# Performance work log

Measured on AMD Instinct MI355X. Metric: run time of the kernel, lower is better.

## Reference

```python
import jax, jax.numpy as jnp
import numpy as np
import math

B, C_LOW, C_HIGH, H, W = 8, 128, 256, 128, 128
KS = 7

def _conv(x, w, b, pad):
    out = jax.lax.conv_general_dilated(
        x, w, window_strides=(1, 1), padding=[(pad, pad), (pad, pad)],
        dimension_numbers=('NCHW', 'OIHW', 'NCHW'))
    return out + b[None, :, None, None]

def setup_inputs() -> dict:
    key = jax.random.key(0)
    ks = jax.random.split(key, 6)
    def he(k, shape):  # matches torch init: normal(0, sqrt(2/(kh*kw*out)))
        n = shape[2] * shape[3] * shape[0]
        return jax.random.normal(k, shape, jnp.float32) * math.sqrt(2.0 / n)
    return {
        'cur_low': jax.random.normal(ks[0], (B, C_LOW, H, W), jnp.float32),
        'key_low': jax.random.normal(ks[1], (B, C_LOW, H, W), jnp.float32),
        'key_high': jax.random.normal(ks[2], (B, C_HIGH, H, W), jnp.float32),
        'w_red': he(ks[3], (256, C_LOW, 3, 3)),
        'b_red': jnp.zeros((256,), jnp.float32),
        'w2': he(ks[4], (256, 512, 3, 3)),
        'b2': jnp.zeros((256,), jnp.float32),
        'w3': he(ks[5], (KS * KS, 256, 1, 1)),
        'b3': jnp.zeros((KS * KS,), jnp.float32),
    }

def reference(cur_low, key_low, key_high, w_red, b_red, w2, b2, w3, b3):
    # KernelWeightPredictor
    cur = jax.nn.relu(_conv(cur_low, w_red, b_red, 1))
    key = jax.nn.relu(_conv(key_low, w_red, b_red, 1))
    x = jax.nn.relu(_conv(jnp.concatenate([cur, key], axis=1), w2, b2, 1))
    x = jax.nn.relu(_conv(x, w3, b3, 0))            # [B, k*k, H, W]
    x = jax.nn.softmax(x, axis=1)
    b, k2, h, w = x.shape
    kernels = jnp.transpose(x, (0, 2, 3, 1)).reshape(b, h, w, KS, KS)
    # SpatiallyVariantConvolution: per-pixel 7x7 kernel applied to key_high
    pad = KS // 2
    fp = jnp.pad(key_high, ((0, 0), (0, 0), (pad, pad), (pad, pad)))
    out = jnp.zeros_like(key_high)
    for i in range(KS):          # fixed 49-iteration unrolled loop; avoids
        for j in range(KS):      # materializing the [B,C,H,W,K,K] patch tensor
            out = out + fp[:, :, i:i + h, j:j + w] * kernels[:, None, :, :, i, j]
    return out
```

## Files before the change

### kernel.cpp

```cpp
#include <hip/hip_runtime.h>
#include <stdint.h>
#include <stddef.h>

#define BN   8
#define HN   128
#define WN   128
#define HP   130
#define CLOW 128
#define CMID 256
#define KO   49

#define KHB_H 134
#define KHB_W 144
#define KHB_PLANE (KHB_H * KHB_W)

typedef __attribute__((ext_vector_type(4))) float f32x4;
typedef __attribute__((ext_vector_type(8))) short bf16x8;

typedef __attribute__((address_space(1))) const uint8_t ga_u8;
typedef __attribute__((address_space(3))) uint8_t lds_u8;

__device__ __forceinline__ short f2bf(float f) {
    uint32_t u = __float_as_uint(f);
    u += 0x7fffu + ((u >> 16) & 1u);
    return (short)(u >> 16);
}
__device__ __forceinline__ float bf2f(short s) {
    return __uint_as_float(((uint32_t)(uint16_t)s) << 16);
}
__device__ __forceinline__ void gload16(const void* g, void* l) {
    __builtin_amdgcn_global_load_lds((ga_u8*)g, (lds_u8*)l, 16, 0, 0);
}

__global__ __launch_bounds__(256) void zero_border_all_kernel(
    short* __restrict__ b0, short* __restrict__ b1,
    short* __restrict__ b2, short* __restrict__ b3) {
    const int which = blockIdx.y;
    short* buf = (which == 0) ? b0 : (which == 1) ? b1 : (which == 2) ? b2 : b3;
    const int gsh = (which < 2) ? 4 : 5;
    const int C = (which < 2) ? 128 : 256;
    int t = blockIdx.x * 256 + threadIdx.x;
    int cell = t >> gsh, g = t & ((1 << gsh) - 1);
    if (cell >= 8 * 516) return;
    int b = cell / 516, r = cell - b * 516;
    int y, x;
    if (r < 260) { y = (r >= 130) ? 129 : 0; x = (r >= 130) ? (r - 130) : r; }
    else { int j = r - 260; y = 1 + (j >> 1); x = (j & 1) ? 129 : 0; }
    uint4 z = {0u, 0u, 0u, 0u};
    *(uint4*)&buf[(((size_t)b * HP + y) * HP + x) * C + g * 8] = z;
}

__global__ __launch_bounds__(256) void convert_pad_kernel(
    const float* __restrict__ src0, const float* __restrict__ src1,
    short* __restrict__ dst0, short* __restrict__ dst1) {
    __shared__ short t[128 * 136];
    const int tid = threadIdx.x;
    const int by = blockIdx.x;
    const int b = by >> 7, y = by & 127;
    const float* src = blockIdx.y ? src1 : src0;
    short* dst = blockIdx.y ? dst1 : dst0;
    #pragma unroll
    for (int k = 0; k < 16; ++k) {
        int slot = k * 256 + tid;
        int c = slot >> 5, xg = slot & 31;
        f32x4 v = *(const f32x4*)&src[(((size_t)b * CLOW + c) * HN + y) * WN + xg * 4];
        #pragma unroll
        for (int j = 0; j < 4; ++j) t[(xg * 4 + j) * 136 + c] = f2bf(v[j]);
    }
    __syncthreads();
    short* drow = dst + (((size_t)b * HP + (y + 1)) * HP + 1) * CLOW;
    #pragma unroll
    for (int k = 0; k < 8; ++k) {
        int slot = k * 256 + tid;
        int x = slot >> 4, cg = slot & 15;
        *(bf16x8*)&drow[x * CLOW + cg * 8] = *(const bf16x8*)&t[x * 136 + cg * 8];
    }
}

__global__ __launch_bounds__(256) void pack_w_all_kernel(
    const float* __restrict__ w1, short* __restrict__ wp1,
    const float* __restrict__ w2, short* __restrict__ wp2,
    const float* __restrict__ w3, short* __restrict__ wp3) {
    int i = blockIdx.x * 256 + threadIdx.x;
    if (i < 256 * 1152 + 256 * 4608) {
        const float* w; short* wp; int CIN, K;
        if (i < 256 * 1152) { w = w1; wp = wp1; CIN = 128; K = 1152; }
        else { i -= 256 * 1152; w = w2; wp = wp2; CIN = 512; K = 4608; }
        int cout = i / K;
        int r = i - cout * K;
        int t = r >> 6;
        int j = r & 63;
        int cb = t / 9;
        int tap = t - cb * 9;
        int cin = cb * 64 + j;
        wp[i] = f2bf(w[((size_t)cout * CIN + cin) * 9 + tap]);
    } else {
        int j = i - (256 * 1152 + 256 * 4608);
        if (j >= 64 * 256) return;
        int o = j >> 8, ch = j & 255;
        wp3[j] = (o < KO) ? f2bf(w3[o * 256 + ch]) : (short)0;
    }
}

template <int CIN, bool OPAD, bool FUSE>
__global__ __launch_bounds__(512, 2) void conv_8ph_kernel(
    const short* __restrict__ in_a, const short* __restrict__ in_b,
    const short* __restrict__ wp, const float* __restrict__ bias,
    short* __restrict__ out_a, short* __restrict__ out_b,
    const short* __restrict__ w3p, const float* __restrict__ b3,
    float* __restrict__ z) {
    constexpr int K = 9 * CIN;
    constexpr int NT = K / 64;
    constexpr bool DUAL = (CIN == 512);
    constexpr int PST = DUAL ? 256 : CIN;
    extern __shared__ __align__(16) short lds[];
    const int tid = threadIdx.x;
    int bx = blockIdx.x;
    bx = (bx & 7) * 64 + (bx >> 3);
    const int b = bx >> 6, y0 = (bx & 63) << 1;
    const short* inA = DUAL ? in_a : (blockIdx.z ? in_b : in_a);
    const short* inB = DUAL ? in_b : inA;
    short* out = (!DUAL && blockIdx.z) ? out_b : out_a;

    const int lane = tid & 63, wv = tid >> 6;
    const int wm = wv >> 2, wn = wv & 3;
    const int lr = lane & 15, lk = lane >> 4;

    const int rA = tid >> 3, cc = tid & 7;
    const int cs = cc ^ (rA & 7);
    const int pthrA0 = rA * PST + cs * 8;
    const int pthrA1 = (rA + 64) * PST + cs * 8;
    const int pthrB0 = rA * K + cs * 8;
    const int pthrB1 = (rA + 64) * K + cs * 8;
    const int dA0 = rA * 64 + cc * 8;
    const int dB0 = rA * 64 + cc * 8;

    const int arow = (wm * 128 + lr) * 64;
    const int brow = (wn * 64 + lr) * 64;
    const int cof0 = ((lk) ^ (lr & 7)) * 8;
    const int cof1 = ((4 + lk) ^ (lr & 7)) * 8;

    f32x4 acc[8][4];
    f32x4 zero = {0.f, 0.f, 0.f, 0.f};
    #pragma unroll
    for (int i = 0; i < 8; ++i)
        #pragma unroll
        for (int j = 0; j < 4; ++j) acc[i][j] = zero;

    auto STAGE2 = [&](int t2, int which, short* bufA, short* bufB) {
        const int cb = (t2 * 57) >> 9;
        const int tap = t2 - cb * 9;
        const int ch0v = cb << 6;
        const short* src = (!DUAL || ch0v < 256) ? inA : inB;
        const int ch0 = DUAL ? (ch0v & 255) : ch0v;
        const int ky = (tap * 11) >> 5;
        const int kx = tap - ky * 3;
        if (which == 0 || which == 2) {
            const int po = (which == 0) ? pthrA0 : pthrA1;
            const int doff = (which == 0) ? 0 : 64 * 64;
            const short* s0 = src + ((size_t)(b * HP + (y0 + ky)) * HP + kx) * PST + ch0;
            gload16(s0 + po, bufA + doff + dA0);
            gload16(s0 + (HP * PST) + po, bufA + 128 * 64 + doff + dA0);
        } else {
            const int h2 = (which == 1) ? 0 : 1;
            const short* sb = wp + (size_t)(h2 * 128) * K + t2 * 64;
            short* d = bufB + h2 * 128 * 64 + dB0;
            gload16(sb + pthrB0, d);
            gload16(sb + pthrB1, d + 64 * 64);
        }
    };

    auto LDA = [&](const short* bufA, int mh, bf16x8 (&a)[4][2]) {
        #pragma unroll
        for (int i = 0; i < 4; ++i) {
            const int ro = arow + (mh * 64 + i * 16) * 64;
            a[i][0] = *(const bf16x8*)(bufA + ro + cof0);
            a[i][1] = *(const bf16x8*)(bufA + ro + cof1);
        }
    };
    auto LDB = [&](const short* bufB, int nh, bf16x8 (&bb)[2][2]) {
        #pragma unroll
        for (int j = 0; j < 2; ++j) {
            const int ro = brow + (nh * 32 + j * 16) * 64;
            bb[j][0] = *(const bf16x8*)(bufB + ro + cof0);
            bb[j][1] = *(const bf16x8*)(bufB + ro + cof1);
        }
    };

#define PH_PRE4() do { __builtin_amdgcn_sched_barrier(0); \
                       __builtin_amdgcn_s_barrier(); \
                       asm volatile("s_waitcnt lgkmcnt(4)" ::: "memory"); \
                       __builtin_amdgcn_sched_barrier(0); \
                       __builtin_amdgcn_s_setprio(1); } while (0)
#define PH_PRE() do { __builtin_amdgcn_sched_barrier(0); \
                      __builtin_amdgcn_s_barrier(); \
                      asm volatile("s_waitcnt lgkmcnt(0)" ::: "memory"); \
                      __builtin_amdgcn_sched_barrier(0); \
                      __builtin_amdgcn_s_setprio(1); } while (0)
#define PH_POST() do { __builtin_amdgcn_s_setprio(0); \
                       __builtin_amdgcn_sched_barrier(0); \
                       __builtin_amdgcn_s_barrier(); } while (0)
#define MFMA_Q(A_, B_, MH, NH) do { \
    _Pragma("unroll") \
    for (int i_ = 0; i_ < 4; ++i_) { \
        _Pragma("unroll") \
        for (int j_ = 0; j_ < 2; ++j_) { \
            acc[(MH)*4+i_][(NH)*2+j_] = __builtin_amdgcn_mfma_f32_16x16x32_bf16( \
                A_[i_][0], B_[j_][0], acc[(MH)*4+i_][(NH)*2+j_], 0, 0, 0); \
            acc[(MH)*4+i_][(NH)*2+j_] = __builtin_amdgcn_mfma_f32_16x16x32_bf16( \
                A_[i_][1], B_[j_][1], acc[(MH)*4+i_][(NH)*2+j_], 0, 0, 0); \
        } \
    } } while (0)

    short* const A0 = lds;
    short* const A1 = lds + 16384;
    short* const B0 = lds + 32768;
    short* const B1 = lds + 49152;

    STAGE2(0, 0, A0, B0); STAGE2(0, 1, A0, B0);
    STAGE2(0, 2, A0, B0); STAGE2(0, 3, A0, B0);
    STAGE2(1, 0, A1, B1); STAGE2(1, 1, A1, B1);
    STAGE2(1, 2, A1, B1); STAGE2(1, 3, A1, B1);
    asm volatile("s_waitcnt vmcnt(8)" ::: "memory");
    __builtin_amdgcn_sched_barrier(0);
    __builtin_amdgcn_s_barrier();

    auto TILE = [&](int t, short* bufA, short* bufB) {
        const int t2 = t + 2;
        const bool st = (t2 < NT);
        bf16x8 ar[4][2], br0[2][2], br1[2][2];
        LDA(bufA, 0, ar);
        LDB(bufB, 0, br0);
        LDB(bufB, 1, br1);
        if (st) STAGE2(t2, 0, bufA, bufB);
        PH_PRE4();
        MFMA_Q(ar, br0, 0, 0);
        PH_POST();
        if (st) STAGE2(t2, 1, bufA, bufB);
        PH_PRE();
        MFMA_Q(ar, br1, 0, 1);
        PH_POST();
        LDA(bufA, 1, ar);
        if (st) STAGE2(t2, 2, bufA, bufB);
        PH_PRE();
        MFMA_Q(ar, br0, 1, 0);
        PH_POST();
        if (st) STAGE2(t2, 3, bufA, bufB);
        PH_PRE();
        MFMA_Q(ar, br1, 1, 1);
        __builtin_amdgcn_s_setprio(0);
        __builtin_amdgcn_sched_barrier(0);
        if (st)                asm volatile("s_waitcnt vmcnt(8)" ::: "memory");
        else if (t == NT - 2)  asm volatile("s_waitcnt vmcnt(0)" ::: "memory");
        __builtin_amdgcn_sched_barrier(0);
        __builtin_amdgcn_s_barrier();
    };

    for (int t = 0; t < NT; t += 2) {
        TILE(t,     A0, B0);
        TILE(t + 1, A1, B1);
    }
#undef PH_PRE4
#undef PH_PRE
#undef PH_POST
#undef MFMA_Q

    float bvs[4];
    #pragma unroll
    for (int nf = 0; nf < 4; ++nf) bvs[nf] = bias[wn * 64 + nf * 16 + lr];

    if constexpr (!FUSE) {
        #pragma unroll
        for (int mf = 0; mf < 8; ++mf) {
            #pragma unroll
            for (int rr = 0; rr < 4; ++rr) {
                const int p = wm * 128 + mf * 16 + lk * 4 + rr;
                const int y = y0 + (p >> 7), x = p & 127;
                short* op;
                if (OPAD)
                    op = out + ((size_t)(b * HP + (y + 1)) * HP + (x + 1)) * CMID + wn * 64 + lr;
                else
                    op = out + ((size_t)((b * HN + y) * WN + x)) * CMID + wn * 64 + lr;
                #pragma unroll
                for (int nf = 0; nf < 4; ++nf)
                    op[nf * 16] = f2bf(fmaxf(acc[mf][nf][rr] + bvs[nf], 0.f));
            }
        }
    } else {
        short* const Xh  = lds;
        short* const W3s = lds + 32768;

        #pragma unroll
        for (int sweep = 0; sweep < 4; ++sweep) {
            const int s = sweep * 512 + tid;
            const int o = s >> 5, c = s & 31;
            gload16(w3p + o * 256 + ((c ^ (o & 7)) << 3), W3s + s * 8);
        }

        const int oo = wn * 16 + lr;
        const float b3v = (oo < KO) ? b3[oo] : 0.f;

        #pragma unroll 1
        for (int r = 0; r < 2; ++r) {
            if (wm == r) {
                #pragma unroll
                for (int nf = 0; nf < 4; ++nf) {
                    const int ch = wn * 64 + nf * 16 + lr;
                    const int ck = ch >> 3, el = ch & 7;
                    #pragma unroll
                    for (int mf = 0; mf < 8; ++mf) {
                        #pragma unroll
                        for (int rr = 0; rr < 4; ++rr) {
                            const int px = mf * 16 + lk * 4 + rr;
                            Xh[px * 256 + ((ck ^ (px & 7)) << 3) + el] =
                                f2bf(fmaxf(acc[mf][nf][rr] + bvs[nf], 0.f));
                        }
                    }
                }
            }
            __syncthreads();
            f32x4 a2[4];
            #pragma unroll
            for (int m = 0; m < 4; ++m) {
                a2[m][0] = b3v; a2[m][1] = b3v; a2[m][2] = b3v; a2[m][3] = b3v;
            }
            #pragma unroll
            for (int ks = 0; ks < 8; ++ks) {
                const bf16x8 bfr =
                    *(const bf16x8*)&W3s[oo * 256 + (((ks * 4 + lk) ^ (oo & 7)) << 3)];
                #pragma unroll
                for (int m = 0; m < 4; ++m) {
                    const int px = wm * 64 + m * 16 + lr;
                    const bf16x8 afr =
                        *(const bf16x8*)&Xh[px * 256 + (((ks * 4 + lk) ^ (px & 7)) << 3)];
                    a2[m] = __builtin_amdgcn_mfma_f32_16x16x32_bf16(afr, bfr, a2[m], 0, 0, 0);
                }
            }
            float* zp = z + ((size_t)(b * 16384 + (y0 + r) * 128)) * 64;
            #pragma unroll
            for (int m = 0; m < 4; ++m) {
                #pragma unroll
                for (int r2 = 0; r2 < 4; ++r2) {
                    const int px = wm * 64 + m * 16 + lk * 4 + r2;
                    zp[px * 64 + oo] = a2[m][r2];
                }
            }
            if (r == 0) __syncthreads();
        }
    }
}

__global__ __launch_bounds__(256) void pad_kh_kernel(
    const float* __restrict__ kh, short* __restrict__ khb) {
    const int bc = blockIdx.x;
    const float* src = kh + (size_t)bc * (HN * WN);
    short* dst = khb + (size_t)bc * KHB_PLANE;
    for (int i = threadIdx.x; i < KHB_H * (KHB_W / 8); i += 256) {
        int yy = i / (KHB_W / 8);
        int g = i - yy * (KHB_W / 8);
        int ys = yy - 3;
        bf16x8 v;
        #pragma unroll
        for (int t = 0; t < 8; ++t) {
            int xs = g * 8 + t - 4;
            float f = 0.f;
            if ((unsigned)ys < 128u && (unsigned)xs < 128u) f = src[(ys << 7) + xs];
            v[t] = f2bf(f);
        }
        *(bf16x8*)&dst[yy * KHB_W + g * 8] = v;
    }
}

__global__ __launch_bounds__(256) void svc4_kernel(
    const float* __restrict__ z, const short* __restrict__ khb,
    float* __restrict__ out) {
    __shared__ float a_s[KO * 64];
    const int tid = threadIdx.x;
    int by = blockIdx.y;
    by = (by & 7) * 128 + (by >> 3);
    const int b = by >> 7, y = by & 127;
    const int x0 = blockIdx.x * 64;

    {
        const int px = tid >> 2, l = tid & 3;
        const float* zp = z + ((size_t)(b * 16384 + (y << 7) + x0 + px)) * 64 + l * 16;
        float v[16];
        #pragma unroll
        for (int q = 0; q < 4; ++q) {
            f32x4 t4 = *(const f32x4*)&zp[q * 4];
            v[q * 4 + 0] = fmaxf(t4[0], 0.f);
            v[q * 4 + 1] = fmaxf(t4[1], 0.f);
            v[q * 4 + 2] = fmaxf(t4[2], 0.f);
            v[q * 4 + 3] = fmaxf(t4[3], 0.f);
        }
        #pragma unroll
        for (int j = 1; j < 16; ++j) if (l == 3) v[j] = -1e30f;
        float m = v[0];
        #pragma unroll
        for (int j = 1; j < 16; ++j) m = fmaxf(m, v[j]);
        m = fmaxf(m, __shfl_xor(m, 1, 64));
        m = fmaxf(m, __shfl_xor(m, 2, 64));
        float s = 0.f;
        #pragma unroll
        for (int j = 0; j < 16; ++j) { v[j] = __expf(v[j] - m); s += v[j]; }
        s += __shfl_xor(s, 1, 64);
        s += __shfl_xor(s, 2, 64);
        const float inv = 1.f / s;
        #pragma unroll
        for (int j = 0; j < 16; ++j) {
            const int o = l * 16 + j;
            if (o < KO) a_s[o * 64 + px] = v[j] * inv;
        }
    }
    __syncthreads();

    const int ci = tid >> 3;
    const int pg = tid & 7;
    const int p0 = x0 + pg * 8;

    float acc[8][8];
    #pragma unroll
    for (int c = 0; c < 8; ++c)
        #pragma unroll
        for (int j = 0; j < 8; ++j) acc[c][j] = 0.f;

    const short* kbase = khb + (((size_t)b * 256 + ci) * KHB_H + y) * KHB_W + p0;

    #pragma unroll 1
    for (int dy = 0; dy < 7; ++dy) {
        f32x4 av[14];
        #pragma unroll
        for (int dx = 0; dx < 7; ++dx) {
            av[dx * 2]     = *(const f32x4*)&a_s[(dy * 7 + dx) * 64 + pg * 8];
            av[dx * 2 + 1] = *(const f32x4*)&a_s[(dy * 7 + dx) * 64 + pg * 8 + 4];
        }
        const short* krow = kbase + dy * KHB_W;
        #pragma unroll
        for (int c = 0; c < 8; ++c) {
            const short* kp = krow + (size_t)c * 32 * KHB_PLANE;
            bf16x8 k0 = *(const bf16x8*)(kp);
            bf16x8 k1 = *(const bf16x8*)(kp + 8);
            float win[16];
            #pragma unroll
            for (int t = 0; t < 8; ++t) { win[t] = bf2f(k0[t]); win[t + 8] = bf2f(k1[t]); }
            #pragma unroll
            for (int dx = 0; dx < 7; ++dx) {
                #pragma unroll
                for (int j = 0; j < 8; ++j)
                    acc[c][j] = fmaf(win[j + dx + 1], av[dx * 2 + (j >> 2)][j & 3],
                                     acc[c][j]);
            }
        }
    }

    #pragma unroll
    for (int c = 0; c < 8; ++c) {
        float* op = out + (((size_t)b * 256 + ci + c * 32) << 14) + (y << 7) + p0;
        f32x4 r0 = {acc[c][0], acc[c][1], acc[c][2], acc[c][3]};
        f32x4 r1 = {acc[c][4], acc[c][5], acc[c][6], acc[c][7]};
        *(f32x4*)op = r0;
        *(f32x4*)(op + 4) = r1;
    }
}

extern "C" void kernel_launch(void* const* d_in, const int* in_sizes, int n_in,
                              void* d_out, int out_size, void* d_ws, size_t ws_size,
                              hipStream_t stream) {
    (void)in_sizes; (void)n_in; (void)out_size; (void)ws_size;
    const float* cur_low  = (const float*)d_in[0];
    const float* key_low  = (const float*)d_in[1];
    const float* key_high = (const float*)d_in[2];
    const float* w_red    = (const float*)d_in[3];
    const float* b_red    = (const float*)d_in[4];
    const float* w2       = (const float*)d_in[5];
    const float* b2       = (const float*)d_in[6];
    const float* w3       = (const float*)d_in[7];
    const float* b3       = (const float*)d_in[8];
    float* out = (float*)d_out;
    char* ws = (char*)d_ws;

    const size_t SZ_XPAD = (size_t)BN * HP * HP * CLOW * 2;
    const size_t SZ_YPAD = (size_t)BN * HP * HP * CMID * 2;
    short* xpadc = (short*)(ws);
    short* xpadk = (short*)(ws + SZ_XPAD);
    short* ypadc = (short*)(ws + 2 * SZ_XPAD);
    short* ypadk = (short*)(ws + 2 * SZ_XPAD + SZ_YPAD);
    short* w1p   = (short*)(ws + 2 * SZ_XPAD + 2 * SZ_YPAD);
    short* w2p   = w1p + (size_t)256 * 1152;
    float* z     = (float*)(ws);
    short* khb   = (short*)(ws + 2 * SZ_XPAD);
    short* w3p   = (short*)((char*)d_out + (size_t)134217728 - 32768);

    hipFuncSetAttribute((const void*)conv_8ph_kernel<128, true, false>,
                        hipFuncAttributeMaxDynamicSharedMemorySize, 131072);
    hipFuncSetAttribute((const void*)conv_8ph_kernel<512, false, true>,
                        hipFuncAttributeMaxDynamicSharedMemorySize, 131072);

    zero_border_all_kernel<<<dim3(516, 4), 256, 0, stream>>>(xpadc, xpadk, ypadc, ypadk);
    convert_pad_kernel<<<dim3(1024, 2), 256, 0, stream>>>(cur_low, key_low, xpadc, xpadk);
    pack_w_all_kernel<<<(256 * (1152 + 4608) + 64 * 256 + 255) / 256, 256, 0, stream>>>(
        w_red, w1p, w2, w2p, w3, w3p);

    conv_8ph_kernel<128, true, false><<<dim3(512, 1, 2), 512, 131072, stream>>>(
        xpadc, xpadk, w1p, b_red, ypadc, ypadk, nullptr, nullptr, nullptr);

    conv_8ph_kernel<512, false, true><<<dim3(512, 1, 1), 512, 131072, stream>>>(
        ypadc, ypadk, w2p, b2, nullptr, nullptr, w3p, b3, z);

    pad_kh_kernel<<<2048, 256, 0, stream>>>(key_high, khb);
    svc4_kernel<<<dim3(2, 1024), 256, 0, stream>>>(z, khb, out);
}
```

Before: 654.5 us.

## Replace ping-pong phased GEMM pipeline with simple one-tile-ahead double buffering

Restructures the MFMA main loop. It drops the 4-phase interleaved schedule, where each tile issued staged global loads for tile t+2 between MFMA quarters with barriers around each phase. The new loop issues all loads for tile t+1 into the other buffer at the start of each tile, waits once, and then runs all MFMAs with only two barriers per tile. This removes six barriers per tile but prefetches only one tile ahead, so global load latency is less hidden behind compute. A __syncthreads is added before the fused epilogue reuses LDS.

```diff
diff --git a/kernel.cpp b/kernel.cpp
--- a/kernel.cpp
+++ b/kernel.cpp
@@ -187,19 +187,6 @@
         }
     };
 
-#define PH_PRE4() do { __builtin_amdgcn_sched_barrier(0); \
-                       __builtin_amdgcn_s_barrier(); \
-                       asm volatile("s_waitcnt lgkmcnt(4)" ::: "memory"); \
-                       __builtin_amdgcn_sched_barrier(0); \
-                       __builtin_amdgcn_s_setprio(1); } while (0)
-#define PH_PRE() do { __builtin_amdgcn_sched_barrier(0); \
-                      __builtin_amdgcn_s_barrier(); \
-                      asm volatile("s_waitcnt lgkmcnt(0)" ::: "memory"); \
-                      __builtin_amdgcn_sched_barrier(0); \
-                      __builtin_amdgcn_s_setprio(1); } while (0)
-#define PH_POST() do { __builtin_amdgcn_s_setprio(0); \
-                       __builtin_amdgcn_sched_barrier(0); \
-                       __builtin_amdgcn_s_barrier(); } while (0)
 #define MFMA_Q(A_, B_, MH, NH) do { \
     _Pragma("unroll") \
     for (int i_ = 0; i_ < 4; ++i_) { \
@@ -219,50 +206,42 @@
 
     STAGE2(0, 0, A0, B0); STAGE2(0, 1, A0, B0);
     STAGE2(0, 2, A0, B0); STAGE2(0, 3, A0, B0);
-    STAGE2(1, 0, A1, B1); STAGE2(1, 1, A1, B1);
-    STAGE2(1, 2, A1, B1); STAGE2(1, 3, A1, B1);
-    asm volatile("s_waitcnt vmcnt(8)" ::: "memory");
-    __builtin_amdgcn_sched_barrier(0);
-    __builtin_amdgcn_s_barrier();
-
-    auto TILE = [&](int t, short* bufA, short* bufB) {
-        const int t2 = t + 2;
-        const bool st = (t2 < NT);
+
+    auto TILE = [&](int t, short* bufA, short* bufB, short* nA, short* nB) {
+        __builtin_amdgcn_s_barrier();
+        __builtin_amdgcn_sched_barrier(0);
+        const int t1 = t + 1;
+        if (t1 < NT) {
+            STAGE2(t1, 0, nA, nB); STAGE2(t1, 1, nA, nB);
+            STAGE2(t1, 2, nA, nB); STAGE2(t1, 3, nA, nB);
+            __builtin_amdgcn_sched_barrier(0);
+            asm volatile("s_waitcnt vmcnt(8)" ::: "memory");
+        } else {
+            __builtin_amdgcn_sched_barrier(0);
+            asm volatile("s_waitcnt vmcnt(0)" ::: "memory");
+        }
+        __builtin_amdgcn_sched_barrier(0);
+        __builtin_amdgcn_s_barrier();
+        __builtin_amdgcn_sched_barrier(0);
         bf16x8 ar[4][2], br0[2][2], br1[2][2];
         LDA(bufA, 0, ar);
         LDB(bufB, 0, br0);
         LDB(bufB, 1, br1);
-        if (st) STAGE2(t2, 0, bufA, bufB);
-        PH_PRE4();
+        __builtin_amdgcn_s_setprio(1);
         MFMA_Q(ar, br0, 0, 0);
-        PH_POST();
-        if (st) STAGE2(t2, 1, bufA, bufB);
-        PH_PRE();
         MFMA_Q(ar, br1, 0, 1);
-        PH_POST();
+        __builtin_amdgcn_s_setprio(0);
         LDA(bufA, 1, ar);
-        if (st) STAGE2(t2, 2, bufA, bufB);
-        PH_PRE();
+        __builtin_amdgcn_s_setprio(1);
         MFMA_Q(ar, br0, 1, 0);
-        PH_POST();
-        if (st) STAGE2(t2, 3, bufA, bufB);
-        PH_PRE();
         MFMA_Q(ar, br1, 1, 1);
         __builtin_amdgcn_s_setprio(0);
-        __builtin_amdgcn_sched_barrier(0);
-        if (st)                asm volatile("s_waitcnt vmcnt(8)" ::: "memory");
-        else if (t == NT - 2)  asm volatile("s_waitcnt vmcnt(0)" ::: "memory");
-        __builtin_amdgcn_sched_barrier(0);
-        __builtin_amdgcn_s_barrier();
     };
 
     for (int t = 0; t < NT; t += 2) {
-        TILE(t,     A0, B0);
-        TILE(t + 1, A1, B1);
-    }
-#undef PH_PRE4
-#undef PH_PRE
-#undef PH_POST
+        TILE(t,     A0, B0, A1, B1);
+        TILE(t + 1, A1, B1, A0, B0);
+    }
 #undef MFMA_Q
 
     float bvs[4];
@@ -287,6 +266,7 @@
             }
         }
     } else {
+        __syncthreads();
         short* const Xh  = lds;
         short* const W3s = lds + 32768;
 
```

Measured after the change: 661.8 us. No clear change (+1.1%).
